# Kernel optimization log

Hardware: AMD Instinct MI355X
Metric: run time of the kernel (lower is better)

Reference implementation:

```python
import jax, jax.numpy as jnp
import numpy as np


def _fexp(x, p):
    # signed power, eps-stabilized so gradients are finite at 0
    return jnp.sign(x) * (jnp.abs(x) + 1e-6) ** p


def _quat_to_rot(q):
    q = q / jnp.linalg.norm(q, axis=-1, keepdims=True)
    w, x, y, z = q[..., 0], q[..., 1], q[..., 2], q[..., 3]
    return jnp.stack([
        jnp.stack([1 - 2 * (y * y + z * z), 2 * (x * y - w * z), 2 * (x * z + w * y)], -1),
        jnp.stack([2 * (x * y + w * z), 1 - 2 * (x * x + z * z), 2 * (y * z - w * x)], -1),
        jnp.stack([2 * (x * z - w * y), 2 * (y * z + w * x), 1 - 2 * (x * x + y * y)], -1),
    ], -2)  # (B,M,3,3)


def _superquadric_points(size, shape, S):
    # size (B,M,3), shape (B,M,2) -> surface samples (B,M,S,3)
    eta = jnp.linspace(-np.pi / 2 + 0.05, np.pi / 2 - 0.05, S, dtype=size.dtype)
    omega = jnp.linspace(-np.pi + 0.05, np.pi - 0.05, S, dtype=size.dtype)
    e1, e2 = shape[..., 0:1], shape[..., 1:2]
    x = size[..., 0:1] * _fexp(jnp.cos(eta), e1) * _fexp(jnp.cos(omega), e2)
    y = size[..., 1:2] * _fexp(jnp.cos(eta), e1) * _fexp(jnp.sin(omega), e2)
    z = size[..., 2:3] * _fexp(jnp.sin(eta), e1)
    return jnp.stack([x, y, z], -1)


def _deform(points, size, deformations):
    # linear tapering along z
    z = points[..., 2]
    fx = deformations[..., 0:1] / size[..., 2:3] * z + 1.0
    fy = deformations[..., 1:2] / size[..., 2:3] * z + 1.0
    return jnp.stack([points[..., 0] * fx, points[..., 1] * fy, z], -1)


def _forward(pcl, translations, rotations, size, shape, deformations, prob, embeddings, S):
    B, N, _ = pcl.shape
    M = translations.shape[1]
    # transform pcl into each primitive-centric frame: (B,N,M,3)
    R = _quat_to_rot(rotations)
    pcl_t = jnp.einsum('bmij,bnmj->bnmi', R, pcl[:, :, None, :] - translations[:, None, :, :])
    # sample + deform superquadric surfaces: (B,M,S,3)
    pts = _deform(_superquadric_points(size, shape, S), size, deformations)
    # gather primitives by argmax over embeddings dim 1
    idx_e = jnp.argmax(embeddings, axis=1)  # (B,M)
    pts = jnp.take_along_axis(pts, idx_e[:, :, None, None], axis=1)
    size_g = jnp.take_along_axis(size, idx_e[:, :, None], axis=1)
    # all-pairs diff / squared distance: (B,M,S,N)
    diff = pts[:, :, :, None, :] - jnp.transpose(pcl_t, (0, 2, 1, 3))[:, :, None, :, :]
    dist = jnp.sum(diff * diff, -1)
    # pcl_to_prim: min over samples, sort over primitives, cumprod coverage
    d1 = jnp.transpose(jnp.min(dist, axis=2), (0, 2, 1))  # (B,N,M)
    order = jnp.argsort(d1, axis=-1)
    distance = jnp.take_along_axis(d1, order, axis=-1)
    probs = jnp.take_along_axis(jnp.broadcast_to(prob[:, None, :], (B, N, M)), order, axis=-1)
    negc = jnp.cumprod(1.0 - probs, axis=-1)
    negc = jnp.concatenate([jnp.ones((B, N, 1), probs.dtype), negc[..., :-1]], -1)
    pcl_to_prim = jnp.sum(distance * probs * negc) / (B * N)
    # prim_to_pcl: min over points, area-weighted mean
    d2 = jnp.min(dist, axis=-1)  # (B,M,S)
    d2 = jnp.where(d2 >= 1e30, 0.0, d2)
    a0, a1, a2 = size_g[..., 0], size_g[..., 1], size_g[..., 2]
    area = 4 * np.pi * ((a0 * a1) ** 1.6 / 3 + (a0 * a2) ** 1.6 / 3 + (a1 * a2) ** 1.6 / 3) ** 0.625
    area = M * area / jnp.sum(area, -1, keepdims=True)
    prim_to_pcl = jnp.sum(jnp.mean(d2, -1) * area) / (B * M)
    # embedding regularizers (prim + 10*tran + discreteness)
    emb_reg = (jnp.mean((jnp.sum(embeddings, 1) - 1.0) ** 2)
               + 10.0 * jnp.mean((jnp.sum(embeddings, 2) - 1.0) ** 2)
               + jnp.mean(embeddings * (1.0 - embeddings)))
    regs = jnp.zeros((), pcl.dtype)  # regularizer_type=None -> all terms zero
    total = pcl_to_prim + prim_to_pcl + regs + emb_reg
    return total, pcl_to_prim, prim_to_pcl, regs, emb_reg


def setup_inputs() -> dict:
    key = jax.random.key(0)
    ks = jax.random.split(key, 8)
    B, N, M, S = 4, 2048, 16, 200
    return {
        'pcl': jax.random.normal(ks[0], (B, N, 3), jnp.float32),
        'translations': 0.2 * jax.random.normal(ks[1], (B, M, 3), jnp.float32),
        'rotations': jax.random.normal(ks[2], (B, M, 4), jnp.float32),
        'size': 0.1 + 0.4 * jax.random.uniform(ks[3], (B, M, 3), jnp.float32),
        'shape': 0.4 + 0.7 * jax.random.uniform(ks[4], (B, M, 2), jnp.float32),
        'deformations': jax.random.uniform(ks[5], (B, M, 2), jnp.float32, -0.5, 0.5),
        'prob': 0.01 + 0.98 * jax.random.uniform(ks[6], (B, M), jnp.float32),
        'embeddings': jax.random.uniform(ks[7], (B, M, M), jnp.float32),
        'n_samples': S,
    }


def reference(pcl, translations, rotations, size, shape, deformations, prob, embeddings, n_samples):
    return _forward(pcl, translations, rotations, size, shape, deformations, prob, embeddings, int(n_samples))
```

## Files before the change

### kernel.cpp

```cpp
#include <hip/hip_runtime.h>
#include <math.h>

#define MAXS 256
#define MM 16

#define INV_2PI 0.15915494309189535f

__device__ __forceinline__ float fpow_(float x, float p) {
    return __builtin_amdgcn_exp2f(p * __builtin_amdgcn_logf(x));
}
__device__ __forceinline__ float fexp_(float v, float p) {
    float s = (v > 0.f) ? 1.f : ((v < 0.f) ? -1.f : 0.f);
    return s * fpow_(fabsf(v) + 1e-6f, p);
}

__global__ void k_main(const float* __restrict__ pcl,
                       const float* __restrict__ trans,
                       const float* __restrict__ rot,
                       const float* __restrict__ size,
                       const float* __restrict__ shapep,
                       const float* __restrict__ defo,
                       const float* __restrict__ emb,
                       const int* __restrict__ Sptr,
                       float* __restrict__ d1,
                       float* __restrict__ d2part,
                       unsigned* __restrict__ counter,
                       int B, int M, int N, int nchunk)
{
    int bm    = blockIdx.x / nchunk;
    int chunk = blockIdx.x - bm*nchunk;
    int b = bm / M, m = bm - b*M;
    int S = min(*Sptr, MAXS);
    int tid = (int)threadIdx.x;

    if (blockIdx.x == 0 && tid == 0) *counter = 0u;

    __shared__ float4 lds_pts[MAXS];
    __shared__ float4 lds_pcl[256];
    __shared__ float  s_R[12];
    __shared__ float  s_par[7];

    if (tid < 64) {
        float v = (tid < 16 && tid < M) ? emb[(size_t)(b*M + tid)*M + m] : -3.4e38f;
        int idx = tid;
        #pragma unroll
        for (int off = 1; off < 16; off <<= 1) {
            float ov = __shfl_xor(v, off, 64);
            int   oi = __shfl_xor(idx, off, 64);
            if (ov > v || (ov == v && oi < idx)) { v = ov; idx = oi; }
        }
        if (tid == 0) {
            const float* sg = size   + (size_t)(b*M + idx)*3;
            const float* sh = shapep + (size_t)(b*M + idx)*2;
            const float* df = defo   + (size_t)(b*M + idx)*2;
            s_par[0]=sg[0]; s_par[1]=sg[1]; s_par[2]=sg[2];
            s_par[3]=sh[0]; s_par[4]=sh[1];
            s_par[5]=df[0]; s_par[6]=df[1];

            const float* q = rot + (size_t)(b*M + m)*4;
            float w=q[0], x=q[1], y=q[2], z=q[3];
            float inv = 1.0f / sqrtf(w*w + x*x + y*y + z*z);
            w*=inv; x*=inv; y*=inv; z*=inv;
            s_R[0] = 1.f - 2.f*(y*y + z*z); s_R[1] = 2.f*(x*y - w*z);       s_R[2] = 2.f*(x*z + w*y);
            s_R[3] = 2.f*(x*y + w*z);       s_R[4] = 1.f - 2.f*(x*x + z*z); s_R[5] = 2.f*(y*z - w*x);
            s_R[6] = 2.f*(x*z - w*y);       s_R[7] = 2.f*(y*z + w*x);       s_R[8] = 1.f - 2.f*(x*x + y*y);
            const float* tr = trans + (size_t)(b*M + m)*3;
            s_R[9] = tr[0]; s_R[10] = tr[1]; s_R[11] = tr[2];
        }
    }
    __syncthreads();

    {
        float sz0 = s_par[0], sz1 = s_par[1], sz2 = s_par[2];
        float e1  = s_par[3], e2  = s_par[4];
        float df0 = s_par[5], df1 = s_par[6];
        double eta0 = -M_PI*0.5 + 0.05, etaE = M_PI*0.5 - 0.05;
        double om0  = -M_PI + 0.05,     omE  = M_PI - 0.05;
        double deta = (S > 1) ? (etaE - eta0) / (double)(S - 1) : 0.0;
        double dom  = (S > 1) ? (omE  - om0)  / (double)(S - 1) : 0.0;
        for (int s = tid; s < S; s += 256) {
            float eta   = (float)(eta0 + s * deta);
            float omega = (float)(om0  + s * dom);
            float se = __builtin_amdgcn_sinf(eta   * INV_2PI);
            float ce = __builtin_amdgcn_cosf(eta   * INV_2PI);
            float so = __builtin_amdgcn_sinf(omega * INV_2PI);
            float co = __builtin_amdgcn_cosf(omega * INV_2PI);
            float fce = fexp_(ce, e1);
            float fse = fexp_(se, e1);
            float fco = fexp_(co, e2);
            float fso = fexp_(so, e2);
            float xx = sz0 * fce * fco;
            float yy = sz1 * fce * fso;
            float zz = sz2 * fse;
            float fx = df0 / sz2 * zz + 1.f;
            float fy = df1 / sz2 * zz + 1.f;
            float px = xx*fx, py = yy*fy, pz = zz;
            lds_pts[s] = make_float4(-2.f*px, -2.f*py, -2.f*pz,
                                     px*px + py*py + pz*pz);
        }
    }

    float R0=s_R[0],R1=s_R[1],R2=s_R[2],R3=s_R[3],R4=s_R[4],R5=s_R[5],
          R6=s_R[6],R7=s_R[7],R8=s_R[8],T0=s_R[9],T1=s_R[10],T2=s_R[11];

    int n0  = chunk * 256;
    int n   = n0 + tid;
    int cnt = min(256, N - n0);

    float qx=0.f, qy=0.f, qz=0.f, h=3.4e38f;
    if (n < N) {
        const float* p = pcl + ((size_t)b*N + n)*3;
        float px = p[0] - T0, py = p[1] - T1, pz = p[2] - T2;
        qx = R0*px + R1*py + R2*pz;
        qy = R3*px + R4*py + R5*pz;
        qz = R6*px + R7*py + R8*pz;
        h  = fmaf(qx,qx, fmaf(qy,qy, qz*qz));
    }
    lds_pcl[tid] = make_float4(qx, qy, qz, h);
    __syncthreads();

    if (n < N) {
        float ma=3.4e38f, mb=3.4e38f, mc=3.4e38f, md=3.4e38f;
        int s = 0;
        for (; s + 3 < S; s += 4) {
            float4 w0 = lds_pts[s+0], w1 = lds_pts[s+1],
                   w2 = lds_pts[s+2], w3 = lds_pts[s+3];
            float t0 = fmaf(w0.x,qx, fmaf(w0.y,qy, fmaf(w0.z,qz, w0.w)));
            float t1 = fmaf(w1.x,qx, fmaf(w1.y,qy, fmaf(w1.z,qz, w1.w)));
            float t2 = fmaf(w2.x,qx, fmaf(w2.y,qy, fmaf(w2.z,qz, w2.w)));
            float t3 = fmaf(w3.x,qx, fmaf(w3.y,qy, fmaf(w3.z,qz, w3.w)));
            ma = fminf(ma, t0); mb = fminf(mb, t1);
            mc = fminf(mc, t2); md = fminf(md, t3);
        }
        for (; s < S; ++s) {
            float4 w0 = lds_pts[s];
            ma = fminf(ma, fmaf(w0.x,qx, fmaf(w0.y,qy, fmaf(w0.z,qz, w0.w))));
        }
        d1[(size_t)bm*N + n] = fminf(fminf(ma, mb), fminf(mc, md)) + h;
    }

    if (tid < S) {
        float4 w = lds_pts[tid];
        float ma=3.4e38f, mb=3.4e38f, mc=3.4e38f, md=3.4e38f;
        int j = 0;
        for (; j + 3 < cnt; j += 4) {
            float4 a = lds_pcl[j+0], bq = lds_pcl[j+1],
                   c = lds_pcl[j+2], dq = lds_pcl[j+3];
            float t0 = fmaf(w.x,a.x,  fmaf(w.y,a.y,  fmaf(w.z,a.z,  a.w)));
            float t1 = fmaf(w.x,bq.x, fmaf(w.y,bq.y, fmaf(w.z,bq.z, bq.w)));
            float t2 = fmaf(w.x,c.x,  fmaf(w.y,c.y,  fmaf(w.z,c.z,  c.w)));
            float t3 = fmaf(w.x,dq.x, fmaf(w.y,dq.y, fmaf(w.z,dq.z, dq.w)));
            ma = fminf(ma, t0); mb = fminf(mb, t1);
            mc = fminf(mc, t2); md = fminf(md, t3);
        }
        for (; j < cnt; ++j) {
            float4 a = lds_pcl[j];
            ma = fminf(ma, fmaf(w.x,a.x, fmaf(w.y,a.y, fmaf(w.z,a.z, a.w))));
        }
        float m2 = fminf(fminf(ma, mb), fminf(mc, md));
        d2part[((size_t)bm*nchunk + chunk)*256 + tid] = m2 + w.w;
    }
}

__device__ __forceinline__ float block_reduce(float v, float* red) {
    int tid = threadIdx.x;
    red[tid] = v; __syncthreads();
    for (int off = 128; off > 0; off >>= 1) {
        if (tid < off) red[tid] += red[tid + off];
        __syncthreads();
    }
    float r = red[0];
    __syncthreads();
    return r;
}

__global__ void k_tail(const float* __restrict__ d1,
                       const float* __restrict__ prob,
                       const float* __restrict__ emb,
                       const float* __restrict__ size,
                       const float* __restrict__ d2part,
                       float* __restrict__ d2min,
                       float* __restrict__ partial1,
                       unsigned* __restrict__ counter,
                       const int* __restrict__ Sptr,
                       float* __restrict__ out,
                       int B, int M, int N, int nb1, int nchunk)
{
    int tid = (int)threadIdx.x;
    int t = blockIdx.x * 256 + tid;
    int S = min(*Sptr, MAXS);
    int BM = B * M;
    __shared__ float red[256];

    float contrib = 0.f;
    if (t < B*N && M == MM) {
        int b = t / N, n = t - b*N;
        float d[MM], p[MM];
        #pragma unroll
        for (int m = 0; m < MM; ++m) {
            d[m] = d1[((size_t)(b*MM + m))*N + n];
            p[m] = prob[b*MM + m];
        }
        #pragma unroll
        for (int m = 0; m < MM; ++m) {
            float prod = p[m];
            #pragma unroll
            for (int mp = 0; mp < MM; ++mp) {
                if (mp == m) continue;
                bool before = (mp < m) ? (d[mp] <= d[m]) : (d[mp] < d[m]);
                prod *= before ? (1.f - p[mp]) : 1.f;
            }
            contrib += d[m] * prod;
        }
    }
    float psum = block_reduce(contrib, red);
    if (tid == 0) partial1[blockIdx.x] = psum;

    int total = BM * 256;
    for (int p = t; p < total; p += nb1 * 256) {
        int pbm = p >> 8, s = p & 255;
        if (s < S) {
            float mn = 3.4e38f;
            #pragma unroll 4
            for (int c = 0; c < nchunk; ++c)
                mn = fminf(mn, d2part[((size_t)pbm*nchunk + c)*256 + s]);
            d2min[p] = mn;
        }
    }

    __threadfence();
    __shared__ int s_last;
    if (tid == 0) s_last = (atomicAdd(counter, 1u) == (unsigned)(nb1 - 1)) ? 1 : 0;
    __syncthreads();
    if (!s_last) return;
    __threadfence();

    float v = 0.f;
    for (int i = tid; i < nb1; i += 256) v += partial1[i];
    float p2p = block_reduce(v, red) / (float)(B * N);

    __shared__ float s_area[256];
    if (tid < BM) {
        int b = tid / M, m = tid - (tid/M)*M;
        int best_i = 0; float best = emb[(size_t)(b*M + 0)*M + m];
        for (int i = 1; i < M; ++i) {
            float e = emb[(size_t)(b*M + i)*M + m];
            if (e > best) { best = e; best_i = i; }
        }
        const float* sg = size + (size_t)(b*M + best_i)*3;
        float a0=sg[0], a1=sg[1], a2=sg[2];
        float pa = fpow_(a0*a1, 1.6f), pb = fpow_(a0*a2, 1.6f), pc = fpow_(a1*a2, 1.6f);
        s_area[tid] = 4.f * 3.14159265358979323846f * fpow_((pa+pb+pc)*(1.f/3.f), 0.625f);
    }
    __syncthreads();

    float contrib2 = 0.f;
    int bm2 = tid >> 2, l = tid & 3;
    if (bm2 < BM) {
        float s2 = 0.f;
        for (int s = l; s < S; s += 4) {
            float dv = d2min[(size_t)bm2*256 + s];
            if (dv < 1e30f) s2 += dv;
        }
        s2 += __shfl_down(s2, 2, 4);
        s2 += __shfl_down(s2, 1, 4);
        if (l == 0) {
            int bb = bm2 / M;
            float sumb = 0.f;
            for (int mp = 0; mp < M; ++mp) sumb += s_area[bb*M + mp];
            float w = (float)M * s_area[bm2] / sumb;
            contrib2 = (s2 / (float)S) * w / (float)BM;
        }
    }
    float prim2pcl = block_reduce((l == 0 && bm2 < BM) ? contrib2 : 0.f, red);

    float a1 = 0.f, a2 = 0.f, a3 = 0.f;
    if (tid < BM) {
        int b = tid / M, m = tid - (tid/M)*M;
        float colsum = 0.f, rowsum = 0.f, ew = 0.f;
        for (int i = 0; i < M; ++i) colsum += emb[(size_t)(b*M + i)*M + m];
        for (int j = 0; j < M; ++j) {
            float e = emb[(size_t)(b*M + m)*M + j];
            rowsum += e;
            ew += e * (1.f - e);
        }
        a1 = (colsum - 1.f) * (colsum - 1.f);
        a2 = (rowsum - 1.f) * (rowsum - 1.f);
        a3 = ew;
    }
    float s1  = block_reduce(a1, red);
    float s2r = block_reduce(a2, red);
    float s3  = block_reduce(a3, red);
    float emb_reg = s1 / (float)BM + 10.f * s2r / (float)BM + s3 / (float)(BM * M);

    if (tid == 0) {
        out[1] = p2p;
        out[2] = prim2pcl;
        out[3] = 0.f;
        out[4] = emb_reg;
        out[0] = p2p + prim2pcl + emb_reg;
    }
}

extern "C" void kernel_launch(void* const* d_in, const int* in_sizes, int n_in,
                              void* d_out, int out_size, void* d_ws, size_t ws_size,
                              hipStream_t stream)
{
    const float* pcl    = (const float*)d_in[0];
    const float* trans  = (const float*)d_in[1];
    const float* rot    = (const float*)d_in[2];
    const float* size   = (const float*)d_in[3];
    const float* shapep = (const float*)d_in[4];
    const float* defo   = (const float*)d_in[5];
    const float* prob   = (const float*)d_in[6];
    const float* emb    = (const float*)d_in[7];
    const int*   Sptr   = (const int*)d_in[8];

    int M = in_sizes[7] / in_sizes[6];
    int B = in_sizes[6] / M;
    int N = in_sizes[0] / (3 * B);
    int BM = B * M;
    int nchunk = (N + 255) / 256;
    int nb1    = (B * N + 255) / 256;

    float* ws = (float*)d_ws;
    size_t off = 0;
    float*    d1       = ws + off; off += (size_t)BM * N;
    float*    d2part   = ws + off; off += (size_t)BM * nchunk * 256;
    float*    d2min    = ws + off; off += (size_t)BM * 256;
    float*    partial1 = ws + off; off += (size_t)nb1;
    off = (off + 3) & ~(size_t)3;
    unsigned* counter  = (unsigned*)(ws + off);

    hipLaunchKernelGGL(k_main, dim3(BM * nchunk), dim3(256), 0, stream,
                       pcl, trans, rot, size, shapep, defo, emb, Sptr,
                       d1, d2part, counter, B, M, N, nchunk);
    hipLaunchKernelGGL(k_tail, dim3(nb1), dim3(256), 0, stream,
                       d1, prob, emb, size, d2part, d2min, partial1, counter,
                       Sptr, (float*)d_out, B, M, N, nb1, nchunk);
}
```

Baseline: 43.54 us.

## Use packed FP32 FMA and min3 with paired SoA LDS layout in distance loops

Splits the LDS sample and point-cloud buffers into paired structure-of-arrays float4s so two candidates share one packed register pair. The inner distance loops then use v_pk_fma_f32 and v_min3_f32 through inline asm, roughly halving the VALU instruction count per pair. Padding entries get a huge sentinel so the loops can run without remainder handling. The d2 loop now always scans 256 points and relies on out-of-range points carrying a max-valued h, which depends on the sentinel and on the loop bound being fixed at 128 pairs.

```diff
diff --git a/kernel.cpp b/kernel.cpp
--- a/kernel.cpp
+++ b/kernel.cpp
@@ -5,6 +5,21 @@
 #define MM 16
 
 #define INV_2PI 0.15915494309189535f
+
+typedef float f32x2 __attribute__((ext_vector_type(2)));
+
+__device__ __forceinline__ f32x2 pk_fma_(f32x2 a, f32x2 b, f32x2 c) {
+    f32x2 d;
+    asm("v_pk_fma_f32 %0, %1, %2, %3" : "=v"(d) : "v"(a), "v"(b), "v"(c));
+    return d;
+}
+__device__ __forceinline__ float min3_(float a, float b, float c) {
+    float d;
+    asm("v_min3_f32 %0, %1, %2, %3" : "=v"(d) : "v"(a), "v"(b), "v"(c));
+    return d;
+}
+
+union F4 { float4 v; f32x2 p[2]; };
 
 __device__ __forceinline__ float fpow_(float x, float p) {
     return __builtin_amdgcn_exp2f(p * __builtin_amdgcn_logf(x));
@@ -35,8 +50,8 @@
 
     if (blockIdx.x == 0 && tid == 0) *counter = 0u;
 
-    __shared__ float4 lds_pts[MAXS];
-    __shared__ float4 lds_pcl[256];
+    __shared__ float4 ldsA[MAXS/2], ldsB[MAXS/2];
+    __shared__ float4 pclA[128], pclB[128];
     __shared__ float  s_R[12];
     __shared__ float  s_par[7];
 
@@ -78,25 +93,33 @@
         double om0  = -M_PI + 0.05,     omE  = M_PI - 0.05;
         double deta = (S > 1) ? (etaE - eta0) / (double)(S - 1) : 0.0;
         double dom  = (S > 1) ? (omE  - om0)  / (double)(S - 1) : 0.0;
-        for (int s = tid; s < S; s += 256) {
-            float eta   = (float)(eta0 + s * deta);
-            float omega = (float)(om0  + s * dom);
-            float se = __builtin_amdgcn_sinf(eta   * INV_2PI);
-            float ce = __builtin_amdgcn_cosf(eta   * INV_2PI);
-            float so = __builtin_amdgcn_sinf(omega * INV_2PI);
-            float co = __builtin_amdgcn_cosf(omega * INV_2PI);
-            float fce = fexp_(ce, e1);
-            float fse = fexp_(se, e1);
-            float fco = fexp_(co, e2);
-            float fso = fexp_(so, e2);
-            float xx = sz0 * fce * fco;
-            float yy = sz1 * fce * fso;
-            float zz = sz2 * fse;
-            float fx = df0 / sz2 * zz + 1.f;
-            float fy = df1 / sz2 * zz + 1.f;
-            float px = xx*fx, py = yy*fy, pz = zz;
-            lds_pts[s] = make_float4(-2.f*px, -2.f*py, -2.f*pz,
-                                     px*px + py*py + pz*pz);
+        int Spad = (S + 3) & ~3;
+        for (int s = tid; s < Spad; s += 256) {
+            float px=0.f, py=0.f, pz=0.f, ps2=3.4e38f;
+            if (s < S) {
+                float eta   = (float)(eta0 + s * deta);
+                float omega = (float)(om0  + s * dom);
+                float se = __builtin_amdgcn_sinf(eta   * INV_2PI);
+                float ce = __builtin_amdgcn_cosf(eta   * INV_2PI);
+                float so = __builtin_amdgcn_sinf(omega * INV_2PI);
+                float co = __builtin_amdgcn_cosf(omega * INV_2PI);
+                float fce = fexp_(ce, e1);
+                float fse = fexp_(se, e1);
+                float fco = fexp_(co, e2);
+                float fso = fexp_(so, e2);
+                float xx = sz0 * fce * fco;
+                float yy = sz1 * fce * fso;
+                float zz = sz2 * fse;
+                float fx = df0 / sz2 * zz + 1.f;
+                float fy = df1 / sz2 * zz + 1.f;
+                px = xx*fx; py = yy*fy; pz = zz;
+                ps2 = px*px + py*py + pz*pz;
+            }
+            int pr = s >> 1, hf = s & 1;
+            ((float*)&ldsA[pr])[hf]     = -2.f*px;
+            ((float*)&ldsA[pr])[2 + hf] = -2.f*py;
+            ((float*)&ldsB[pr])[hf]     = -2.f*pz;
+            ((float*)&ldsB[pr])[2 + hf] = ps2;
         }
     }
 
@@ -105,7 +128,6 @@
 
     int n0  = chunk * 256;
     int n   = n0 + tid;
-    int cnt = min(256, N - n0);
 
     float qx=0.f, qy=0.f, qz=0.f, h=3.4e38f;
     if (n < N) {
@@ -116,49 +138,57 @@
         qz = R6*px + R7*py + R8*pz;
         h  = fmaf(qx,qx, fmaf(qy,qy, qz*qz));
     }
-    lds_pcl[tid] = make_float4(qx, qy, qz, h);
+    {
+        int pr = tid >> 1, hf = tid & 1;
+        ((float*)&pclA[pr])[hf]     = qx;
+        ((float*)&pclA[pr])[2 + hf] = qy;
+        ((float*)&pclB[pr])[hf]     = qz;
+        ((float*)&pclB[pr])[2 + hf] = h;
+    }
     __syncthreads();
 
     if (n < N) {
-        float ma=3.4e38f, mb=3.4e38f, mc=3.4e38f, md=3.4e38f;
-        int s = 0;
-        for (; s + 3 < S; s += 4) {
-            float4 w0 = lds_pts[s+0], w1 = lds_pts[s+1],
-                   w2 = lds_pts[s+2], w3 = lds_pts[s+3];
-            float t0 = fmaf(w0.x,qx, fmaf(w0.y,qy, fmaf(w0.z,qz, w0.w)));
-            float t1 = fmaf(w1.x,qx, fmaf(w1.y,qy, fmaf(w1.z,qz, w1.w)));
-            float t2 = fmaf(w2.x,qx, fmaf(w2.y,qy, fmaf(w2.z,qz, w2.w)));
-            float t3 = fmaf(w3.x,qx, fmaf(w3.y,qy, fmaf(w3.z,qz, w3.w)));
-            ma = fminf(ma, t0); mb = fminf(mb, t1);
-            mc = fminf(mc, t2); md = fminf(md, t3);
-        }
-        for (; s < S; ++s) {
-            float4 w0 = lds_pts[s];
-            ma = fminf(ma, fmaf(w0.x,qx, fmaf(w0.y,qy, fmaf(w0.z,qz, w0.w))));
-        }
-        d1[(size_t)bm*N + n] = fminf(fminf(ma, mb), fminf(mc, md)) + h;
+        f32x2 qx2 = {qx,qx}, qy2 = {qy,qy}, qz2 = {qz,qz};
+        float ma = 3.4e38f, mb = 3.4e38f;
+        int npair = (S + 1) >> 1;
+        int np2 = npair & ~1;
+        int j = 0;
+        for (; j < np2; j += 2) {
+            F4 A0, B0, A1, B1;
+            A0.v = ldsA[j];   B0.v = ldsB[j];
+            A1.v = ldsA[j+1]; B1.v = ldsB[j+1];
+            f32x2 t0 = pk_fma_(A0.p[0], qx2, pk_fma_(A0.p[1], qy2, pk_fma_(B0.p[0], qz2, B0.p[1])));
+            f32x2 t1 = pk_fma_(A1.p[0], qx2, pk_fma_(A1.p[1], qy2, pk_fma_(B1.p[0], qz2, B1.p[1])));
+            ma = min3_(ma, t0.x, t0.y);
+            mb = min3_(mb, t1.x, t1.y);
+        }
+        for (; j < npair; ++j) {
+            F4 A0, B0; A0.v = ldsA[j]; B0.v = ldsB[j];
+            f32x2 t0 = pk_fma_(A0.p[0], qx2, pk_fma_(A0.p[1], qy2, pk_fma_(B0.p[0], qz2, B0.p[1])));
+            ma = min3_(ma, t0.x, t0.y);
+        }
+        d1[(size_t)bm*N + n] = fminf(ma, mb) + h;
     }
 
     if (tid < S) {
-        float4 w = lds_pts[tid];
-        float ma=3.4e38f, mb=3.4e38f, mc=3.4e38f, md=3.4e38f;
-        int j = 0;
-        for (; j + 3 < cnt; j += 4) {
-            float4 a = lds_pcl[j+0], bq = lds_pcl[j+1],
-                   c = lds_pcl[j+2], dq = lds_pcl[j+3];
-            float t0 = fmaf(w.x,a.x,  fmaf(w.y,a.y,  fmaf(w.z,a.z,  a.w)));
-            float t1 = fmaf(w.x,bq.x, fmaf(w.y,bq.y, fmaf(w.z,bq.z, bq.w)));
-            float t2 = fmaf(w.x,c.x,  fmaf(w.y,c.y,  fmaf(w.z,c.z,  c.w)));
-            float t3 = fmaf(w.x,dq.x, fmaf(w.y,dq.y, fmaf(w.z,dq.z, dq.w)));
-            ma = fminf(ma, t0); mb = fminf(mb, t1);
-            mc = fminf(mc, t2); md = fminf(md, t3);
-        }
-        for (; j < cnt; ++j) {
-            float4 a = lds_pcl[j];
-            ma = fminf(ma, fmaf(w.x,a.x, fmaf(w.y,a.y, fmaf(w.z,a.z, a.w))));
-        }
-        float m2 = fminf(fminf(ma, mb), fminf(mc, md));
-        d2part[((size_t)bm*nchunk + chunk)*256 + tid] = m2 + w.w;
+        int pr = tid >> 1, hf = tid & 1;
+        float m2x = ((const float*)&ldsA[pr])[hf];
+        float m2y = ((const float*)&ldsA[pr])[2 + hf];
+        float m2z = ((const float*)&ldsB[pr])[hf];
+        float pw2 = ((const float*)&ldsB[pr])[2 + hf];
+        f32x2 px2 = {m2x,m2x}, py2 = {m2y,m2y}, pz2 = {m2z,m2z};
+        float ma = 3.4e38f, mb = 3.4e38f;
+        #pragma unroll 2
+        for (int j = 0; j < 128; j += 2) {
+            F4 A0, B0, A1, B1;
+            A0.v = pclA[j];   B0.v = pclB[j];
+            A1.v = pclA[j+1]; B1.v = pclB[j+1];
+            f32x2 t0 = pk_fma_(A0.p[0], px2, pk_fma_(A0.p[1], py2, pk_fma_(B0.p[0], pz2, B0.p[1])));
+            f32x2 t1 = pk_fma_(A1.p[0], px2, pk_fma_(A1.p[1], py2, pk_fma_(B1.p[0], pz2, B1.p[1])));
+            ma = min3_(ma, t0.x, t0.y);
+            mb = min3_(mb, t1.x, t1.y);
+        }
+        d2part[((size_t)bm*nchunk + chunk)*256 + tid] = fminf(ma, mb) + pw2;
     }
 }
 
```

Result: faster. 40.55 us (-6.9%).
